# Kernel optimization log

Measured on AMD Instinct MI355X. Metric: run time of the kernel, lower is better.

The kernel has to match this reference:

```python
import jax, jax.numpy as jnp
import numpy as np

N_CLIN = 38
N_PIX = 36
N_NODES = N_CLIN + N_PIX  # 74
FV = 128
B = 1024
HID = 512
N_OUT = 1


def _base_edges():
    # Faithful to Network.get_edges: self-edges for all nodes, then for each
    # pixel node i, bidirectional edges to every clinical node.
    ids = np.arange(N_NODES)
    parts = [np.stack([ids, ids])]
    c = np.arange(N_CLIN)
    for i in range(N_CLIN, N_NODES):
        ii = np.full(N_CLIN, i)
        parts.append(np.stack([ii, c]))
        parts.append(np.stack([c, ii]))
    return np.concatenate(parts, axis=1)  # (2, 2810)


def setup_inputs() -> dict:
    key = jax.random.key(0)
    ks = jax.random.split(key, 10)
    base = _base_edges()  # (2, E0)
    # Batched edge index: per-sample copy offset by ind*N_NODES (batch-major order,
    # matching the torch.cat loop).
    offs = np.arange(B)[None, :, None] * N_NODES  # (1, B, 1)
    edge_index = (base[:, None, :] + offs).reshape(2, -1)  # (2, B*E0)
    s = 1.0 / np.sqrt(FV)
    return {
        "clinical_embeddings": jax.random.normal(ks[0], (B, N_CLIN, FV), jnp.float32),
        "image_embeddings": jax.random.normal(ks[1], (B, N_PIX, FV), jnp.float32),
        # RMRM graph-net params (single message-passing layer, fv_dim -> fv_dim)
        "W_self": jax.random.normal(ks[2], (FV, FV), jnp.float32) * s,
        "W_msg": jax.random.normal(ks[3], (FV, FV), jnp.float32) * s,
        "b_g": jnp.zeros((FV,), jnp.float32),
        # OutputBlock MLP params: fv_dim*(n_clinical+1)=4992 -> 512 -> 1
        "W1": jax.random.normal(ks[4], (FV * (N_CLIN + 1), HID), jnp.float32) * (1.0 / np.sqrt(FV * (N_CLIN + 1))),
        "b1": jnp.zeros((HID,), jnp.float32),
        "W2": jax.random.normal(ks[5], (HID, N_OUT), jnp.float32) * (1.0 / np.sqrt(HID)),
        "b2": jnp.zeros((N_OUT,), jnp.float32),
        "edge_index": jnp.asarray(edge_index, jnp.int32),
    }


def reference(clinical_embeddings, image_embeddings, W_self, W_msg, b_g, W1, b1, W2, b2, edge_index):
    # Assemble node features: [B, n_nodes, fv] -> flat [B*n_nodes, fv]
    x = jnp.concatenate([clinical_embeddings, image_embeddings], axis=1)
    x = x.reshape(-1, FV)
    src, dst = edge_index[0], edge_index[1]
    n_total = B * N_NODES
    # Mean-aggregated message passing (RMRM layer): gather + segment-sum
    msg = jax.ops.segment_sum(x[src], dst, num_segments=n_total)  # [B*N, FV]
    deg = jax.ops.segment_sum(jnp.ones_like(src, jnp.float32), dst, num_segments=n_total)
    agg = msg / deg[:, None]
    h = jax.nn.relu(x @ W_self + agg @ W_msg + b_g)  # [B*N, FV]
    h = h.reshape(B, N_NODES, FV)
    graph_fvs_c = h[:, :N_CLIN]          # [B, 38, FV]
    graph_fvs_i = h[:, N_CLIN:]          # [B, 36, FV]
    # AvgPool2d(6,6) over [B, FV, 6, 6] == mean over the 36 pixel nodes
    gap = graph_fvs_i.mean(axis=1)       # [B, FV]
    combined = jnp.concatenate([graph_fvs_c, gap[:, None, :]], axis=1).reshape(B, -1)
    # OutputBlock MLP
    out = jax.nn.relu(combined @ W1 + b1) @ W2 + b2  # [B, 1]
    return out
```

## Files before the change

kernel.cpp:

```cpp
#include <hip/hip_runtime.h>

#define FV 128
#define NCLIN 38
#define NPIX 36
#define BATCH 1024
#define HID 512
#define COMB 4992

typedef __attribute__((ext_vector_type(4))) float f32x4;
typedef __attribute__((ext_vector_type(8))) short s16x8;

#define WS_WCT  0
#define WS_WIT  8192
#define WS_TC   16384
#define WS_TI   147456
#define WS_COMB 278528
#define WS_W1T  2834432
#define WS_Z    4112384

__device__ __forceinline__ unsigned short bf16_rne(float f) {
    union { float f; unsigned int u; } v; v.f = f;
    unsigned int u = v.u;
    u += 0x7fffu + ((u >> 16) & 1u);
    return (unsigned short)(u >> 16);
}

__device__ __forceinline__ s16x8 load8_bf16(const float* __restrict__ p) {
    const float4 v0 = *(const float4*)p;
    const float4 v1 = *(const float4*)(p + 4);
    union { unsigned short u[8]; s16x8 v; } r;
    r.u[0] = bf16_rne(v0.x); r.u[1] = bf16_rne(v0.y);
    r.u[2] = bf16_rne(v0.z); r.u[3] = bf16_rne(v0.w);
    r.u[4] = bf16_rne(v1.x); r.u[5] = bf16_rne(v1.y);
    r.u[6] = bf16_rne(v1.z); r.u[7] = bf16_rne(v1.w);
    return r.v;
}

__global__ __launch_bounds__(128) void k_prep(
    const float* __restrict__ clin, const float* __restrict__ img,
    const float* __restrict__ wself, const float* __restrict__ wmsg,
    const float* __restrict__ bg, float* __restrict__ ws)
{
    const int b = blockIdx.x;
    const int f = threadIdx.x;
    if (b >= BATCH) {
        const int r = b - BATCH;
        const int idx = r * 128 + f;
        const float wm = wmsg[idx];
        const float s  = wself[idx];
        unsigned short* WcT = (unsigned short*)(ws + WS_WCT);
        unsigned short* WiT = (unsigned short*)(ws + WS_WIT);
        WcT[f * 128 + r] = bf16_rne(s + wm * (1.0f / 37.0f));
        WiT[f * 128 + r] = bf16_rne(s + wm * (1.0f / 39.0f));
        return;
    }
    __shared__ float lc[128];
    __shared__ float li[128];
    float sc = 0.f, si = 0.f;
    const float* xc = clin + (size_t)b * NCLIN * FV + f;
#pragma unroll
    for (int n = 0; n < NCLIN; ++n) sc += xc[n * FV];
    const float* xi = img + (size_t)b * NPIX * FV + f;
#pragma unroll
    for (int n = 0; n < NPIX; ++n) si += xi[n * FV];
    lc[f] = sc * (1.0f / 39.0f);
    li[f] = si * (1.0f / 37.0f);
    __syncthreads();
    const float bgv = bg[f];
    float tc = bgv, ti = bgv;
#pragma unroll 4
    for (int k = 0; k < 128; ++k) {
        const float wm = wmsg[k * 128 + f];
        tc += li[k] * wm;
        ti += lc[k] * wm;
    }
    ws[WS_TC + b * 128 + f] = tc;
    ws[WS_TI + b * 128 + f] = ti;
}

__global__ __launch_bounds__(256) void k_nodes_mfma(
    const float* __restrict__ clin, const float* __restrict__ img,
    float* __restrict__ ws)
{
    const int b     = blockIdx.x;
    const int phase = blockIdx.y;
    const int NN    = phase ? NPIX : NCLIN;
    const float* x  = phase ? (img + (size_t)b * NPIX * FV)
                            : (clin + (size_t)b * NCLIN * FV);
    const unsigned short* WT =
        (const unsigned short*)(ws + (phase ? WS_WIT : WS_WCT));
    const float* tv = ws + (phase ? WS_TI : WS_TC) + b * 128;
    unsigned short* combined =
        (unsigned short*)(ws + WS_COMB) + (size_t)b * COMB;

    const int t    = threadIdx.x;
    const int wave = t >> 6;
    const int lane = t & 63;
    const int l16  = lane & 15;
    const int q    = lane >> 4;

    const int r0 = (l16      < NN) ? l16      : (NN - 1);
    const int r1 = (16 + l16 < NN) ? 16 + l16 : (NN - 1);
    const int r2 = (32 + l16 < NN) ? 32 + l16 : (NN - 1);
    const int n0 = wave * 32 + l16;

    f32x4 acc[3][2] = {};

#pragma unroll
    for (int kk = 0; kk < 4; ++kk) {
        const int ko = kk * 32 + q * 8;
        const s16x8 a0 = load8_bf16(x + r0 * 128 + ko);
        const s16x8 a1 = load8_bf16(x + r1 * 128 + ko);
        const s16x8 a2 = load8_bf16(x + r2 * 128 + ko);
        const s16x8 b0 = *(const s16x8*)&WT[(n0)      * 128 + ko];
        const s16x8 b1 = *(const s16x8*)&WT[(n0 + 16) * 128 + ko];
        acc[0][0] = __builtin_amdgcn_mfma_f32_16x16x32_bf16(a0, b0, acc[0][0], 0, 0, 0);
        acc[0][1] = __builtin_amdgcn_mfma_f32_16x16x32_bf16(a0, b1, acc[0][1], 0, 0, 0);
        acc[1][0] = __builtin_amdgcn_mfma_f32_16x16x32_bf16(a1, b0, acc[1][0], 0, 0, 0);
        acc[1][1] = __builtin_amdgcn_mfma_f32_16x16x32_bf16(a1, b1, acc[1][1], 0, 0, 0);
        acc[2][0] = __builtin_amdgcn_mfma_f32_16x16x32_bf16(a2, b0, acc[2][0], 0, 0, 0);
        acc[2][1] = __builtin_amdgcn_mfma_f32_16x16x32_bf16(a2, b1, acc[2][1], 0, 0, 0);
    }

    const float t0 = tv[wave * 32 + l16];
    const float t1 = tv[wave * 32 + 16 + l16];

    if (phase == 0) {
#pragma unroll
        for (int rt = 0; rt < 3; ++rt) {
#pragma unroll
            for (int r = 0; r < 4; ++r) {
                const int node = rt * 16 + q * 4 + r;
                if (node < NCLIN) {
                    combined[node * 128 + wave * 32 + l16] =
                        bf16_rne(fmaxf(acc[rt][0][r] + t0, 0.f));
                    combined[node * 128 + wave * 32 + 16 + l16] =
                        bf16_rne(fmaxf(acc[rt][1][r] + t1, 0.f));
                }
            }
        }
    } else {
        float g0 = 0.f, g1 = 0.f;
#pragma unroll
        for (int rt = 0; rt < 3; ++rt) {
#pragma unroll
            for (int r = 0; r < 4; ++r) {
                const int node = rt * 16 + q * 4 + r;
                if (node < NPIX) {
                    g0 += fmaxf(acc[rt][0][r] + t0, 0.f);
                    g1 += fmaxf(acc[rt][1][r] + t1, 0.f);
                }
            }
        }
        g0 += __shfl_xor(g0, 16); g0 += __shfl_xor(g0, 32);
        g1 += __shfl_xor(g1, 16); g1 += __shfl_xor(g1, 32);
        if (q == 0) {
            combined[NCLIN * 128 + wave * 32 + l16] =
                bf16_rne(g0 * (1.0f / 36.0f));
            combined[NCLIN * 128 + wave * 32 + 16 + l16] =
                bf16_rne(g1 * (1.0f / 36.0f));
        }
    }
}

__global__ __launch_bounds__(256) void k_w1t(
    const float* __restrict__ W1, float* __restrict__ ws)
{
    unsigned short* W1T = (unsigned short*)(ws + WS_W1T);
    const int k0 = blockIdx.x * 64;
    const int n0 = blockIdx.y * 64;
    __shared__ float tile[64][65];
    const int t   = threadIdx.x;
    const int r16 = t >> 4;
    const int c4  = (t & 15) * 4;
#pragma unroll
    for (int p = 0; p < 4; ++p) {
        const int r = p * 16 + r16;
        const float4 v = *(const float4*)&W1[(size_t)(k0 + r) * HID + n0 + c4];
        tile[r][c4 + 0] = v.x; tile[r][c4 + 1] = v.y;
        tile[r][c4 + 2] = v.z; tile[r][c4 + 3] = v.w;
    }
    __syncthreads();
    const int j  = t >> 2;
    const int i0 = (t & 3) * 16;
    unsigned short tmp[16];
#pragma unroll
    for (int s = 0; s < 16; ++s) tmp[s] = bf16_rne(tile[i0 + s][j]);
    unsigned short* dst = &W1T[(size_t)(n0 + j) * COMB + k0 + i0];
    *(uint4*)&dst[0] = *(uint4*)&tmp[0];
    *(uint4*)&dst[8] = *(uint4*)&tmp[8];
}

__global__ __launch_bounds__(256) void k_gemm_mfma(float* __restrict__ ws)
{
    const unsigned short* Abase = (const unsigned short*)(ws + WS_COMB);
    const unsigned short* Bbase = (const unsigned short*)(ws + WS_W1T);
    const int m0    = blockIdx.x * 64;
    const int n0    = blockIdx.y * 64;
    const int ks    = blockIdx.z;
    const int kbase = ks * 1248;
    float* Z = ws + WS_Z + (size_t)ks * (BATCH * HID);

    __shared__ __align__(16) unsigned short As[64 * 40];
    __shared__ __align__(16) unsigned short Bs[64 * 40];

    const int t    = threadIdx.x;
    const int wave = t >> 6;
    const int lane = t & 63;
    const int wm   = (wave & 1) * 32;
    const int wn   = (wave >> 1) * 32;
    const int l16  = lane & 15;
    const int q    = lane >> 4;

    const int sr = t >> 2;
    const int sc = (t & 3) * 8;

    f32x4 acc00 = {}, acc01 = {}, acc10 = {}, acc11 = {};

    for (int kb = 0; kb < 1248; kb += 32) {
        __syncthreads();
        const int kk = kbase + kb + sc;
        *(uint4*)&As[sr * 40 + sc] =
            *(const uint4*)&Abase[(size_t)(m0 + sr) * COMB + kk];
        *(uint4*)&Bs[sr * 40 + sc] =
            *(const uint4*)&Bbase[(size_t)(n0 + sr) * COMB + kk];
        __syncthreads();

        const s16x8 a0 = *(const s16x8*)&As[(wm + l16) * 40 + q * 8];
        const s16x8 a1 = *(const s16x8*)&As[(wm + 16 + l16) * 40 + q * 8];
        const s16x8 b0 = *(const s16x8*)&Bs[(wn + l16) * 40 + q * 8];
        const s16x8 b1 = *(const s16x8*)&Bs[(wn + 16 + l16) * 40 + q * 8];

        acc00 = __builtin_amdgcn_mfma_f32_16x16x32_bf16(a0, b0, acc00, 0, 0, 0);
        acc01 = __builtin_amdgcn_mfma_f32_16x16x32_bf16(a0, b1, acc01, 0, 0, 0);
        acc10 = __builtin_amdgcn_mfma_f32_16x16x32_bf16(a1, b0, acc10, 0, 0, 0);
        acc11 = __builtin_amdgcn_mfma_f32_16x16x32_bf16(a1, b1, acc11, 0, 0, 0);
    }

    const int rbase = q * 4;
#pragma unroll
    for (int r = 0; r < 4; ++r) {
        const int mr0 = m0 + wm + rbase + r;
        Z[(size_t)(mr0)      * HID + n0 + wn +      l16] = acc00[r];
        Z[(size_t)(mr0)      * HID + n0 + wn + 16 + l16] = acc01[r];
        Z[(size_t)(mr0 + 16) * HID + n0 + wn +      l16] = acc10[r];
        Z[(size_t)(mr0 + 16) * HID + n0 + wn + 16 + l16] = acc11[r];
    }
}

__global__ __launch_bounds__(64) void k_out(
    const float* __restrict__ b1, const float* __restrict__ W2,
    const float* __restrict__ b2, const float* __restrict__ ws,
    float* __restrict__ out)
{
    const int b = blockIdx.x;
    const int l = threadIdx.x;
    const float* z0 = ws + WS_Z + (size_t)b * HID;
    const float* z1 = z0 + BATCH * HID;
    const float* z2 = z1 + BATCH * HID;
    const float* z3 = z2 + BATCH * HID;
    float s = 0.f;
#pragma unroll
    for (int j = 0; j < 8; ++j) {
        const int h = l + j * 64;
        float z = z0[h] + z1[h] + z2[h] + z3[h] + b1[h];
        z = fmaxf(z, 0.f);
        s += z * W2[h];
    }
#pragma unroll
    for (int off = 32; off > 0; off >>= 1) s += __shfl_down(s, off);
    if (l == 0) out[b] = s + b2[0];
}

extern "C" void kernel_launch(void* const* d_in, const int* in_sizes, int n_in,
                              void* d_out, int out_size, void* d_ws, size_t ws_size,
                              hipStream_t stream) {
    const float* clin  = (const float*)d_in[0];
    const float* img   = (const float*)d_in[1];
    const float* wself = (const float*)d_in[2];
    const float* wmsg  = (const float*)d_in[3];
    const float* bg    = (const float*)d_in[4];
    const float* W1    = (const float*)d_in[5];
    const float* b1    = (const float*)d_in[6];
    const float* W2    = (const float*)d_in[7];
    const float* b2    = (const float*)d_in[8];
    float* ws  = (float*)d_ws;
    float* out = (float*)d_out;

    k_w1t <<<dim3(78, 8), 256, 0, stream>>>(W1, ws);
    k_prep<<<dim3(BATCH + 128), 128, 0, stream>>>(clin, img, wself, wmsg, bg, ws);
    k_nodes_mfma<<<dim3(BATCH, 2), 256, 0, stream>>>(clin, img, ws);
    k_gemm_mfma<<<dim3(16, 8, 4), 256, 0, stream>>>(ws);
    k_out<<<dim3(BATCH), 64, 0, stream>>>(b1, W2, b2, ws, out);
}
```

Before: 177.0 us.

## Fuse per-batch prep and node MFMA into one kernel staging inputs in LDS

Merges the per-sample mean and message-bias computation with the node MFMA kernel, so each block loads its 74x128 node features once, converts them to bf16 in padded shared memory, and reuses them for both the sums and the MFMA operands. The W1 transpose and the combined-weight construction now share one launch, removing a launch and the intermediate TC/TI workspace round trip. The costs are larger shared-memory use per block and fewer blocks. The node sums are now taken from bf16-rounded values, which slightly changes numerics.

New measurement: 160.0 us. 1.11x faster.

```diff
diff --git a/kernel.cpp b/kernel.cpp
--- a/kernel.cpp
+++ b/kernel.cpp
@@ -3,20 +3,20 @@
 #define FV 128
 #define NCLIN 38
 #define NPIX 36
+#define NTOT 74
 #define BATCH 1024
 #define HID 512
 #define COMB 4992
+#define XPAD 136
 
 typedef __attribute__((ext_vector_type(4))) float f32x4;
 typedef __attribute__((ext_vector_type(8))) short s16x8;
 
 #define WS_WCT  0
 #define WS_WIT  8192
-#define WS_TC   16384
-#define WS_TI   147456
-#define WS_COMB 278528
-#define WS_W1T  2834432
-#define WS_Z    4112384
+#define WS_COMB 16384
+#define WS_W1T  2572288
+#define WS_Z    3850240
 
 __device__ __forceinline__ unsigned short bf16_rne(float f) {
     union { float f; unsigned int u; } v; v.f = f;
@@ -24,153 +24,36 @@
     u += 0x7fffu + ((u >> 16) & 1u);
     return (unsigned short)(u >> 16);
 }
-
-__device__ __forceinline__ s16x8 load8_bf16(const float* __restrict__ p) {
-    const float4 v0 = *(const float4*)p;
-    const float4 v1 = *(const float4*)(p + 4);
-    union { unsigned short u[8]; s16x8 v; } r;
-    r.u[0] = bf16_rne(v0.x); r.u[1] = bf16_rne(v0.y);
-    r.u[2] = bf16_rne(v0.z); r.u[3] = bf16_rne(v0.w);
-    r.u[4] = bf16_rne(v1.x); r.u[5] = bf16_rne(v1.y);
-    r.u[6] = bf16_rne(v1.z); r.u[7] = bf16_rne(v1.w);
-    return r.v;
-}
-
-__global__ __launch_bounds__(128) void k_prep(
-    const float* __restrict__ clin, const float* __restrict__ img,
-    const float* __restrict__ wself, const float* __restrict__ wmsg,
-    const float* __restrict__ bg, float* __restrict__ ws)
+__device__ __forceinline__ float bf2f(unsigned short h) {
+    union { unsigned int u; float f; } v; v.u = ((unsigned int)h) << 16;
+    return v.f;
+}
+
+__global__ __launch_bounds__(256) void k_static(
+    const float* __restrict__ W1, const float* __restrict__ wself,
+    const float* __restrict__ wmsg, float* __restrict__ ws)
 {
-    const int b = blockIdx.x;
-    const int f = threadIdx.x;
-    if (b >= BATCH) {
-        const int r = b - BATCH;
-        const int idx = r * 128 + f;
-        const float wm = wmsg[idx];
-        const float s  = wself[idx];
+    const int t = threadIdx.x;
+    if (blockIdx.x == 78) {
         unsigned short* WcT = (unsigned short*)(ws + WS_WCT);
         unsigned short* WiT = (unsigned short*)(ws + WS_WIT);
-        WcT[f * 128 + r] = bf16_rne(s + wm * (1.0f / 37.0f));
-        WiT[f * 128 + r] = bf16_rne(s + wm * (1.0f / 39.0f));
+        const int r  = blockIdx.y * 16 + (t >> 4);
+        const int f0 = (t & 15) * 8;
+#pragma unroll
+        for (int j = 0; j < 8; ++j) {
+            const int f = f0 + j;
+            const int idx = r * 128 + f;
+            const float wm = wmsg[idx];
+            const float s  = wself[idx];
+            WcT[f * 128 + r] = bf16_rne(s + wm * (1.0f / 37.0f));
+            WiT[f * 128 + r] = bf16_rne(s + wm * (1.0f / 39.0f));
+        }
         return;
     }
-    __shared__ float lc[128];
-    __shared__ float li[128];
-    float sc = 0.f, si = 0.f;
-    const float* xc = clin + (size_t)b * NCLIN * FV + f;
-#pragma unroll
-    for (int n = 0; n < NCLIN; ++n) sc += xc[n * FV];
-    const float* xi = img + (size_t)b * NPIX * FV + f;
-#pragma unroll
-    for (int n = 0; n < NPIX; ++n) si += xi[n * FV];
-    lc[f] = sc * (1.0f / 39.0f);
-    li[f] = si * (1.0f / 37.0f);
-    __syncthreads();
-    const float bgv = bg[f];
-    float tc = bgv, ti = bgv;
-#pragma unroll 4
-    for (int k = 0; k < 128; ++k) {
-        const float wm = wmsg[k * 128 + f];
-        tc += li[k] * wm;
-        ti += lc[k] * wm;
-    }
-    ws[WS_TC + b * 128 + f] = tc;
-    ws[WS_TI + b * 128 + f] = ti;
-}
-
-__global__ __launch_bounds__(256) void k_nodes_mfma(
-    const float* __restrict__ clin, const float* __restrict__ img,
-    float* __restrict__ ws)
-{
-    const int b     = blockIdx.x;
-    const int phase = blockIdx.y;
-    const int NN    = phase ? NPIX : NCLIN;
-    const float* x  = phase ? (img + (size_t)b * NPIX * FV)
-                            : (clin + (size_t)b * NCLIN * FV);
-    const unsigned short* WT =
-        (const unsigned short*)(ws + (phase ? WS_WIT : WS_WCT));
-    const float* tv = ws + (phase ? WS_TI : WS_TC) + b * 128;
-    unsigned short* combined =
-        (unsigned short*)(ws + WS_COMB) + (size_t)b * COMB;
-
-    const int t    = threadIdx.x;
-    const int wave = t >> 6;
-    const int lane = t & 63;
-    const int l16  = lane & 15;
-    const int q    = lane >> 4;
-
-    const int r0 = (l16      < NN) ? l16      : (NN - 1);
-    const int r1 = (16 + l16 < NN) ? 16 + l16 : (NN - 1);
-    const int r2 = (32 + l16 < NN) ? 32 + l16 : (NN - 1);
-    const int n0 = wave * 32 + l16;
-
-    f32x4 acc[3][2] = {};
-
-#pragma unroll
-    for (int kk = 0; kk < 4; ++kk) {
-        const int ko = kk * 32 + q * 8;
-        const s16x8 a0 = load8_bf16(x + r0 * 128 + ko);
-        const s16x8 a1 = load8_bf16(x + r1 * 128 + ko);
-        const s16x8 a2 = load8_bf16(x + r2 * 128 + ko);
-        const s16x8 b0 = *(const s16x8*)&WT[(n0)      * 128 + ko];
-        const s16x8 b1 = *(const s16x8*)&WT[(n0 + 16) * 128 + ko];
-        acc[0][0] = __builtin_amdgcn_mfma_f32_16x16x32_bf16(a0, b0, acc[0][0], 0, 0, 0);
-        acc[0][1] = __builtin_amdgcn_mfma_f32_16x16x32_bf16(a0, b1, acc[0][1], 0, 0, 0);
-        acc[1][0] = __builtin_amdgcn_mfma_f32_16x16x32_bf16(a1, b0, acc[1][0], 0, 0, 0);
-        acc[1][1] = __builtin_amdgcn_mfma_f32_16x16x32_bf16(a1, b1, acc[1][1], 0, 0, 0);
-        acc[2][0] = __builtin_amdgcn_mfma_f32_16x16x32_bf16(a2, b0, acc[2][0], 0, 0, 0);
-        acc[2][1] = __builtin_amdgcn_mfma_f32_16x16x32_bf16(a2, b1, acc[2][1], 0, 0, 0);
-    }
-
-    const float t0 = tv[wave * 32 + l16];
-    const float t1 = tv[wave * 32 + 16 + l16];
-
-    if (phase == 0) {
-#pragma unroll
-        for (int rt = 0; rt < 3; ++rt) {
-#pragma unroll
-            for (int r = 0; r < 4; ++r) {
-                const int node = rt * 16 + q * 4 + r;
-                if (node < NCLIN) {
-                    combined[node * 128 + wave * 32 + l16] =
-                        bf16_rne(fmaxf(acc[rt][0][r] + t0, 0.f));
-                    combined[node * 128 + wave * 32 + 16 + l16] =
-                        bf16_rne(fmaxf(acc[rt][1][r] + t1, 0.f));
-                }
-            }
-        }
-    } else {
-        float g0 = 0.f, g1 = 0.f;
-#pragma unroll
-        for (int rt = 0; rt < 3; ++rt) {
-#pragma unroll
-            for (int r = 0; r < 4; ++r) {
-                const int node = rt * 16 + q * 4 + r;
-                if (node < NPIX) {
-                    g0 += fmaxf(acc[rt][0][r] + t0, 0.f);
-                    g1 += fmaxf(acc[rt][1][r] + t1, 0.f);
-                }
-            }
-        }
-        g0 += __shfl_xor(g0, 16); g0 += __shfl_xor(g0, 32);
-        g1 += __shfl_xor(g1, 16); g1 += __shfl_xor(g1, 32);
-        if (q == 0) {
-            combined[NCLIN * 128 + wave * 32 + l16] =
-                bf16_rne(g0 * (1.0f / 36.0f));
-            combined[NCLIN * 128 + wave * 32 + 16 + l16] =
-                bf16_rne(g1 * (1.0f / 36.0f));
-        }
-    }
-}
-
-__global__ __launch_bounds__(256) void k_w1t(
-    const float* __restrict__ W1, float* __restrict__ ws)
-{
     unsigned short* W1T = (unsigned short*)(ws + WS_W1T);
     const int k0 = blockIdx.x * 64;
     const int n0 = blockIdx.y * 64;
     __shared__ float tile[64][65];
-    const int t   = threadIdx.x;
     const int r16 = t >> 4;
     const int c4  = (t & 15) * 4;
 #pragma unroll
@@ -189,6 +72,144 @@
     unsigned short* dst = &W1T[(size_t)(n0 + j) * COMB + k0 + i0];
     *(uint4*)&dst[0] = *(uint4*)&tmp[0];
     *(uint4*)&dst[8] = *(uint4*)&tmp[8];
+}
+
+__global__ __launch_bounds__(256) void k_batch(
+    const float* __restrict__ clin, const float* __restrict__ img,
+    const float* __restrict__ wmsg, const float* __restrict__ bg,
+    float* __restrict__ ws)
+{
+    const int b = blockIdx.x;
+    const int t = threadIdx.x;
+
+    __shared__ __align__(16) unsigned short xl[NTOT * XPAD];
+    __shared__ float lc[128];
+    __shared__ float li[128];
+    __shared__ float tcv[128];
+    __shared__ float tiv[128];
+
+    const float* xc = clin + (size_t)b * NCLIN * FV;
+    const float* xi = img  + (size_t)b * NPIX * FV;
+    for (int i = t; i < NCLIN * 32; i += 256) {
+        const int row = i >> 5, c4 = (i & 31) * 4;
+        const float4 v = *(const float4*)&xc[row * 128 + c4];
+        ushort4 u;
+        u.x = bf16_rne(v.x); u.y = bf16_rne(v.y);
+        u.z = bf16_rne(v.z); u.w = bf16_rne(v.w);
+        *(ushort4*)&xl[row * XPAD + c4] = u;
+    }
+    for (int i = t; i < NPIX * 32; i += 256) {
+        const int row = i >> 5, c4 = (i & 31) * 4;
+        const float4 v = *(const float4*)&xi[row * 128 + c4];
+        ushort4 u;
+        u.x = bf16_rne(v.x); u.y = bf16_rne(v.y);
+        u.z = bf16_rne(v.z); u.w = bf16_rne(v.w);
+        *(ushort4*)&xl[(NCLIN + row) * XPAD + c4] = u;
+    }
+    __syncthreads();
+
+    const int f = t & 127;
+    if (t < 128) {
+        float s = 0.f;
+#pragma unroll
+        for (int n = 0; n < NCLIN; ++n) s += bf2f(xl[n * XPAD + f]);
+        lc[f] = s * (1.0f / 39.0f);
+    } else {
+        float s = 0.f;
+#pragma unroll
+        for (int n = 0; n < NPIX; ++n) s += bf2f(xl[(NCLIN + n) * XPAD + f]);
+        li[f] = s * (1.0f / 37.0f);
+    }
+    __syncthreads();
+
+    {
+        const float* src = (t < 128) ? li : lc;
+        float acc = bg[f];
+#pragma unroll 4
+        for (int k = 0; k < 128; ++k) acc += src[k] * wmsg[k * 128 + f];
+        if (t < 128) tcv[f] = acc; else tiv[f] = acc;
+    }
+    __syncthreads();
+
+    const unsigned short* WcT = (const unsigned short*)(ws + WS_WCT);
+    const unsigned short* WiT = (const unsigned short*)(ws + WS_WIT);
+    unsigned short* combined =
+        (unsigned short*)(ws + WS_COMB) + (size_t)b * COMB;
+
+    const int wave = t >> 6;
+    const int lane = t & 63;
+    const int l16  = lane & 15;
+    const int q    = lane >> 4;
+    const int n0   = wave * 32 + l16;
+
+#pragma unroll
+    for (int phase = 0; phase < 2; ++phase) {
+        const int NN   = phase ? NPIX : NCLIN;
+        const int xoff = phase ? NCLIN : 0;
+        const unsigned short* WT = phase ? WiT : WcT;
+        const float* tvv = phase ? tiv : tcv;
+
+        const int r0 = xoff + ((l16      < NN) ? l16      : (NN - 1));
+        const int r1 = xoff + ((16 + l16 < NN) ? 16 + l16 : (NN - 1));
+        const int r2 = xoff + ((32 + l16 < NN) ? 32 + l16 : (NN - 1));
+
+        f32x4 acc[3][2] = {};
+#pragma unroll
+        for (int kk = 0; kk < 4; ++kk) {
+            const int ko = kk * 32 + q * 8;
+            const s16x8 a0 = *(const s16x8*)&xl[r0 * XPAD + ko];
+            const s16x8 a1 = *(const s16x8*)&xl[r1 * XPAD + ko];
+            const s16x8 a2 = *(const s16x8*)&xl[r2 * XPAD + ko];
+            const s16x8 b0 = *(const s16x8*)&WT[(n0)      * 128 + ko];
+            const s16x8 b1 = *(const s16x8*)&WT[(n0 + 16) * 128 + ko];
+            acc[0][0] = __builtin_amdgcn_mfma_f32_16x16x32_bf16(a0, b0, acc[0][0], 0, 0, 0);
+            acc[0][1] = __builtin_amdgcn_mfma_f32_16x16x32_bf16(a0, b1, acc[0][1], 0, 0, 0);
+            acc[1][0] = __builtin_amdgcn_mfma_f32_16x16x32_bf16(a1, b0, acc[1][0], 0, 0, 0);
+            acc[1][1] = __builtin_amdgcn_mfma_f32_16x16x32_bf16(a1, b1, acc[1][1], 0, 0, 0);
+            acc[2][0] = __builtin_amdgcn_mfma_f32_16x16x32_bf16(a2, b0, acc[2][0], 0, 0, 0);
+            acc[2][1] = __builtin_amdgcn_mfma_f32_16x16x32_bf16(a2, b1, acc[2][1], 0, 0, 0);
+        }
+
+        const float t0 = tvv[wave * 32 + l16];
+        const float t1 = tvv[wave * 32 + 16 + l16];
+
+        if (phase == 0) {
+#pragma unroll
+            for (int rt = 0; rt < 3; ++rt) {
+#pragma unroll
+                for (int r = 0; r < 4; ++r) {
+                    const int node = rt * 16 + q * 4 + r;
+                    if (node < NCLIN) {
+                        combined[node * 128 + wave * 32 + l16] =
+                            bf16_rne(fmaxf(acc[rt][0][r] + t0, 0.f));
+                        combined[node * 128 + wave * 32 + 16 + l16] =
+                            bf16_rne(fmaxf(acc[rt][1][r] + t1, 0.f));
+                    }
+                }
+            }
+        } else {
+            float g0 = 0.f, g1 = 0.f;
+#pragma unroll
+            for (int rt = 0; rt < 3; ++rt) {
+#pragma unroll
+                for (int r = 0; r < 4; ++r) {
+                    const int node = rt * 16 + q * 4 + r;
+                    if (node < NPIX) {
+                        g0 += fmaxf(acc[rt][0][r] + t0, 0.f);
+                        g1 += fmaxf(acc[rt][1][r] + t1, 0.f);
+                    }
+                }
+            }
+            g0 += __shfl_xor(g0, 16); g0 += __shfl_xor(g0, 32);
+            g1 += __shfl_xor(g1, 16); g1 += __shfl_xor(g1, 32);
+            if (q == 0) {
+                combined[NCLIN * 128 + wave * 32 + l16] =
+                    bf16_rne(g0 * (1.0f / 36.0f));
+                combined[NCLIN * 128 + wave * 32 + 16 + l16] =
+                    bf16_rne(g1 * (1.0f / 36.0f));
+            }
+        }
+    }
 }
 
 __global__ __launch_bounds__(256) void k_gemm_mfma(float* __restrict__ ws)
@@ -287,9 +308,8 @@
     float* ws  = (float*)d_ws;
     float* out = (float*)d_out;
 
-    k_w1t <<<dim3(78, 8), 256, 0, stream>>>(W1, ws);
-    k_prep<<<dim3(BATCH + 128), 128, 0, stream>>>(clin, img, wself, wmsg, bg, ws);
-    k_nodes_mfma<<<dim3(BATCH, 2), 256, 0, stream>>>(clin, img, ws);
+    k_static<<<dim3(79, 8), 256, 0, stream>>>(W1, wself, wmsg, ws);
+    k_batch <<<dim3(BATCH), 256, 0, stream>>>(clin, img, wmsg, bg, ws);
     k_gemm_mfma<<<dim3(16, 8, 4), 256, 0, stream>>>(ws);
     k_out<<<dim3(BATCH), 64, 0, stream>>>(b1, W2, b2, ws, out);
 }
```
